# Optimization experiments

Hardware: AMD Instinct MI355X
Metric: run time of the kernel (lower is better)

## Reference

```python
import jax, jax.numpy as jnp
import numpy as np

N_NODES = 100000
N_EDGES = 1000000
D = 128          # node_dim == out_dim (embedding_dim)
EDGE_DIM = 10
NEG_SLOPE = 0.01  # torch leaky_relu default
EPS = 1e-16       # PyG softmax denominator eps


def _leaky(x):
    return jnp.where(x >= 0, x, NEG_SLOPE * x)


def setup_inputs() -> dict:
    key = jax.random.key(0)
    ks = jax.random.split(key, 12)
    s = lambda fan_in: 1.0 / np.sqrt(fan_in)
    return {
        "x": jax.random.normal(ks[0], (N_NODES, D), jnp.float32),
        "edge_index": jax.random.randint(ks[1], (2, N_EDGES), 0, N_NODES),
        "edge_attr": jax.random.normal(ks[2], (N_EDGES, EDGE_DIM), jnp.float32),
        # q: Linear(D, D, bias=False)
        "Wq": jax.random.uniform(ks[3], (D, D), jnp.float32, -s(D), s(D)),
        # k: Linear(EDGE_DIM, D, bias=False)
        "Wk": jax.random.uniform(ks[4], (D, EDGE_DIM), jnp.float32, -s(EDGE_DIM), s(EDGE_DIM)),
        # v: Linear(EDGE_DIM, D) with bias
        "Wv": jax.random.uniform(ks[5], (D, EDGE_DIM), jnp.float32, -s(EDGE_DIM), s(EDGE_DIM)),
        "bv": jax.random.uniform(ks[6], (D,), jnp.float32, -s(EDGE_DIM), s(EDGE_DIM)),
        # attn_score_layer: Linear(2D, D) -> ReLU -> Linear(D, 1)
        "W1": jax.random.uniform(ks[7], (D, 2 * D), jnp.float32, -s(2 * D), s(2 * D)),
        "b1": jax.random.uniform(ks[8], (D,), jnp.float32, -s(2 * D), s(2 * D)),
        "W2": jax.random.uniform(ks[9], (1, D), jnp.float32, -s(D), s(D)),
        "b2": jax.random.uniform(ks[10], (1,), jnp.float32, -s(D), s(D)),
    }


def reference(x, edge_index, edge_attr, Wq, Wk, Wv, bv, W1, b1, W2, b2):
    N = x.shape[0]
    tgt = edge_index[1]                       # destination node per edge [E]
    q = x @ Wq.T                              # [N, D] node queries
    x_i = q[tgt]                              # gather target queries [E, D]
    k = _leaky(edge_attr @ Wk.T)              # [E, D]
    v = _leaky(edge_attr @ Wv.T + bv)         # [E, D]
    h = jnp.concatenate([x_i, k], axis=-1)    # [E, 2D]
    scores = (jax.nn.relu(h @ W1.T + b1) @ W2.T + b2)[:, 0]  # [E]
    # segment softmax over edges grouped by target node (PyG softmax)
    smax = jax.ops.segment_max(scores, tgt, num_segments=N)  # [N]
    e = jnp.exp(scores - smax[tgt])
    denom = jax.ops.segment_sum(e, tgt, num_segments=N)
    attn = e / (denom[tgt] + EPS)             # [E]
    out = jax.ops.segment_sum(v * attn[:, None], tgt, num_segments=N)  # [N, D]
    return out, attn
```

## Files before the change

kernel.cpp:

```cpp
#include <hip/hip_runtime.h>
#include <stdint.h>

#define NN 100000
#define NE 1000000
#define NTILES (NE / 64)
#define NB_SCAN 391

typedef __attribute__((ext_vector_type(8))) short bf16x8;
typedef __attribute__((ext_vector_type(4))) float f32x4;

static const size_t OFF_W1K   = 0;
static const size_t OFF_W1BP  = 8192;
static const size_t OFF_MTB   = 40960;
static const size_t OFF_RP    = 73728;
static const size_t OFF_CUR   = 524288;
static const size_t OFF_PART  = 1048576;
static const size_t OFF_BSUM  = 1572864;
static const size_t OFF_BSUMX = 1576960;
static const size_t OFF_CNT   = 1581056;
static const size_t OFF_PT    = 2097152;
static const size_t OFF_EVALS = 10485760;
static const size_t OFF_EAS   = 14485760;
static const size_t OFF_SNODE = 34485760;

__device__ inline unsigned short f2bf(float f) {
    const unsigned int u = __float_as_uint(f);
    return (unsigned short)((u + 0x7fffu + ((u >> 16) & 1u)) >> 16);
}

__device__ inline unsigned int cvtpk(float lo, float hi) {
    unsigned int r;
    asm("v_cvt_pk_bf16_f32 %0, %1, %2" : "=v"(r) : "v"(lo), "v"(hi));
    return r;
}

__device__ inline float lk(float v) {
    return fmaxf(v, 0.f) + 0.01f * fminf(v, 0.f);
}

union BU { bf16x8 v; uint4 u; };

__global__ __launch_bounds__(128) void prep_kernel(
    const float* __restrict__ W1, const float* __restrict__ Wq,
    const float* __restrict__ Wk,
    unsigned short* __restrict__ w1k, unsigned short* __restrict__ w1bp,
    unsigned short* __restrict__ mtb)
{
    const int l = blockIdx.x;
    const int i = threadIdx.x;
    float acc = 0.f;
#pragma unroll 8
    for (int j = 0; j < 128; ++j)
        acc = fmaf(W1[i * 256 + j], Wq[j * 128 + l], acc);
    mtb[i * 128 + l] = f2bf(acc);
    if (i < 32)
        w1k[l * 32 + i] = (i < 10) ? f2bf(Wk[l * 10 + i]) : (unsigned short)0;
    const int m = l;
    const int j = (m & ~31) + 16 * ((m >> 2) & 1) + 4 * ((m >> 3) & 3) + (m & 3);
    w1bp[i * 128 + m] = f2bf(W1[i * 256 + 128 + j]);
}

__global__ __launch_bounds__(256) void node_score_kernel(
    const float* __restrict__ x, const unsigned short* __restrict__ mtb_g,
    const float* __restrict__ b1, unsigned short* __restrict__ s_node)
{
    __shared__ __align__(16) unsigned short mt_s[128 * 136];
    const int t = threadIdx.x;
    for (int idx = t; idx < 2048; idx += 256) {
        const uint4 v = ((const uint4*)mtb_g)[idx];
        const int row = idx >> 4, q = idx & 15;
        *(uint4*)&mt_s[row * 136 + q * 8] = v;
    }
    __syncthreads();

    const int lane = t & 63;
    const int wave = t >> 6;
    const int h    = lane >> 4;
    const int e15  = lane & 15;
    const int node = blockIdx.x * 64 + wave * 16 + e15;
    const int nc   = min(node, NN - 1);
    const int lds_base = e15 * 136 + h * 8;

    const f32x4 z4 = {0.f, 0.f, 0.f, 0.f};
    f32x4 acc[8];
#pragma unroll
    for (int g = 0; g < 8; ++g) acc[g] = z4;

#pragma unroll
    for (int s = 0; s < 4; ++s) {
        const float4 xa = *(const float4*)&x[(size_t)nc * 128 + s * 32 + h * 8];
        const float4 xb = *(const float4*)&x[(size_t)nc * 128 + s * 32 + h * 8 + 4];
        BU bx;
        bx.u.x = cvtpk(xa.x, xa.y);
        bx.u.y = cvtpk(xa.z, xa.w);
        bx.u.z = cvtpk(xb.x, xb.y);
        bx.u.w = cvtpk(xb.z, xb.w);
#pragma unroll
        for (int g = 0; g < 8; ++g) {
            const bf16x8 a = *(const bf16x8*)&mt_s[lds_base + g * (16 * 136) + s * 32];
            acc[g] = __builtin_amdgcn_mfma_f32_16x16x32_bf16(a, bx.v, acc[g], 0, 0, 0);
        }
    }

    if (node < NN) {
#pragma unroll
        for (int g = 0; g < 8; ++g) {
            const float4 bb = *(const float4*)&b1[g * 16 + h * 4];
            uint2 o2;
            o2.x = cvtpk(acc[g][0] + bb.x, acc[g][1] + bb.y);
            o2.y = cvtpk(acc[g][2] + bb.z, acc[g][3] + bb.w);
            *(uint2*)&s_node[(size_t)node * 128 + g * 16 + h * 4] = o2;
        }
    }
}

__global__ __launch_bounds__(256) void hist_kernel(
    const int* __restrict__ tgt, int* __restrict__ cnt)
{
    const int e = blockIdx.x * 256 + threadIdx.x;
    if (e < NE) atomicAdd(&cnt[tgt[e]], 1);
}

__global__ __launch_bounds__(256) void scan1_kernel(
    const int* __restrict__ cnt, int* __restrict__ part, int* __restrict__ bsum)
{
    __shared__ int s[256];
    const int t = threadIdx.x;
    const int idx = blockIdx.x * 256 + t;
    const int v = (idx < NN) ? cnt[idx] : 0;
    s[t] = v;
    __syncthreads();
    for (int off = 1; off < 256; off <<= 1) {
        const int u = (t >= off) ? s[t - off] : 0;
        __syncthreads();
        s[t] += u;
        __syncthreads();
    }
    part[idx] = s[t] - v;
    if (t == 255) bsum[blockIdx.x] = s[255];
}

__global__ __launch_bounds__(512) void scan2_kernel(
    const int* __restrict__ bsum, int* __restrict__ bsumx)
{
    __shared__ int s[512];
    const int t = threadIdx.x;
    const int v = (t < NB_SCAN) ? bsum[t] : 0;
    s[t] = v;
    __syncthreads();
    for (int off = 1; off < 512; off <<= 1) {
        const int u = (t >= off) ? s[t - off] : 0;
        __syncthreads();
        s[t] += u;
        __syncthreads();
    }
    if (t < NB_SCAN) bsumx[t] = s[t] - v;
}

__global__ __launch_bounds__(256) void scan3_kernel(
    const int* __restrict__ part, const int* __restrict__ bsumx,
    int* __restrict__ rowptr, int* __restrict__ cursor)
{
    const int idx = blockIdx.x * 256 + threadIdx.x;
    if (idx < NN) {
        const int rp = part[idx] + bsumx[idx >> 8];
        rowptr[idx] = rp;
        cursor[idx] = rp;
    }
    if (idx == 0) rowptr[NN] = NE;
}

__global__ __launch_bounds__(256) void fill_kernel(
    const int* __restrict__ tgt, int* __restrict__ cursor, int2* __restrict__ pt)
{
    const int e = blockIdx.x * 256 + threadIdx.x;
    if (e < NE) {
        const int tg = tgt[e];
        const int p  = atomicAdd(&cursor[tg], 1);
        pt[p] = make_int2(e, tg);
    }
}

__global__ __launch_bounds__(256) void edge_kernel(
    const float* __restrict__ edge_attr, const int2* __restrict__ pt,
    const unsigned short* __restrict__ w1k_g, const unsigned short* __restrict__ w1bp_g,
    const float* __restrict__ W2, const float* __restrict__ b2,
    const unsigned short* __restrict__ s_node,
    float* __restrict__ e_vals, unsigned int* __restrict__ eas)
{
    __shared__ __align__(16) unsigned short w1b_s[128 * 136];

    const int t = threadIdx.x;
    for (int idx = t; idx < 2048; idx += 256) {
        const uint4 v = ((const uint4*)w1bp_g)[idx];
        const int row = idx >> 4, q = idx & 15;
        *(uint4*)&w1b_s[row * 136 + q * 8] = v;
    }

    const int lane = t & 63;
    const int wave = t >> 6;
    const int h    = lane >> 4;
    const int e15  = lane & 15;

    bf16x8 a1[8];
#pragma unroll
    for (int f = 0; f < 8; ++f)
        a1[f] = *(const bf16x8*)&w1k_g[(f * 16 + e15) * 32 + h * 8];
    const float b2v = b2[0];

    __syncthreads();

    const int lds_base = e15 * 136 + h * 8;
    const int cstep    = gridDim.x * 64;

    int c = blockIdx.x * 64 + wave * 16 + e15;

    int2 ptc = pt[min(c, NE - 1)];
    int2 ptn = pt[min(c + cstep, NE - 1)];

    uint2 sn[8];
#pragma unroll
    for (int g = 0; g < 8; ++g)
        sn[g] = *(const uint2*)&s_node[(size_t)ptc.y * 128 + g * 16 + h * 4];

    float ea0 = 0.f, ea1 = 0.f, ea2 = 0.f, ea3 = 0.f, ea4 = 0.f;
    float ea5 = 0.f, ea6 = 0.f, ea7 = 0.f, ea8 = 0.f, ea9 = 0.f;
    {
        const float* pa = edge_attr + (size_t)ptc.x * 10;
        if (h == 0) {
            const float2 u0 = *(const float2*)(pa + 0);
            const float2 u1 = *(const float2*)(pa + 2);
            const float2 u2 = *(const float2*)(pa + 4);
            const float2 u3 = *(const float2*)(pa + 6);
            ea0 = u0.x; ea1 = u0.y; ea2 = u1.x; ea3 = u1.y;
            ea4 = u2.x; ea5 = u2.y; ea6 = u3.x; ea7 = u3.y;
        } else if (h == 1) {
            const float2 u4 = *(const float2*)(pa + 8);
            ea8 = u4.x; ea9 = u4.y;
        }
    }

    for (int tile = blockIdx.x; tile < NTILES; tile += gridDim.x, c += cstep) {
        const int2 ptn2 = pt[min(c + 2 * cstep, NE - 1)];
        uint2 sn_n[8];
#pragma unroll
        for (int g = 0; g < 8; ++g)
            sn_n[g] = *(const uint2*)&s_node[(size_t)ptn.y * 128 + g * 16 + h * 4];
        float en0 = 0.f, en1 = 0.f, en2 = 0.f, en3 = 0.f, en4 = 0.f;
        float en5 = 0.f, en6 = 0.f, en7 = 0.f, en8 = 0.f, en9 = 0.f;
        {
            const float* pa = edge_attr + (size_t)ptn.x * 10;
            if (h == 0) {
                const float2 u0 = *(const float2*)(pa + 0);
                const float2 u1 = *(const float2*)(pa + 2);
                const float2 u2 = *(const float2*)(pa + 4);
                const float2 u3 = *(const float2*)(pa + 6);
                en0 = u0.x; en1 = u0.y; en2 = u1.x; en3 = u1.y;
                en4 = u2.x; en5 = u2.y; en6 = u3.x; en7 = u3.y;
            } else if (h == 1) {
                const float2 u4 = *(const float2*)(pa + 8);
                en8 = u4.x; en9 = u4.y;
            }
        }

        bf16x8 b1 = (bf16x8){0, 0, 0, 0, 0, 0, 0, 0};
        {
            unsigned int* po = eas + (size_t)c * 5;
            if (h == 0) {
                BU bu;
                bu.u.x = cvtpk(ea0, ea1);
                bu.u.y = cvtpk(ea2, ea3);
                bu.u.z = cvtpk(ea4, ea5);
                bu.u.w = cvtpk(ea6, ea7);
                b1 = bu.v;
                po[0] = bu.u.x; po[1] = bu.u.y; po[2] = bu.u.z; po[3] = bu.u.w;
            } else if (h == 1) {
                BU bu;
                bu.u.x = cvtpk(ea8, ea9);
                bu.u.y = 0; bu.u.z = 0; bu.u.w = 0;
                b1 = bu.v;
                po[4] = bu.u.x;
            }
        }

        const f32x4 z4 = {0.f, 0.f, 0.f, 0.f};
        f32x4 acc1[8];
#pragma unroll
        for (int f = 0; f < 8; ++f)
            acc1[f] = __builtin_amdgcn_mfma_f32_16x16x32_bf16(a1[f], b1, z4, 0, 0, 0);

        bf16x8 pb[4];
#pragma unroll
        for (int s = 0; s < 4; ++s) {
            BU bu;
            bu.u.x = cvtpk(lk(acc1[2 * s][0]), lk(acc1[2 * s][1]));
            bu.u.y = cvtpk(lk(acc1[2 * s][2]), lk(acc1[2 * s][3]));
            bu.u.z = cvtpk(lk(acc1[2 * s + 1][0]), lk(acc1[2 * s + 1][1]));
            bu.u.w = cvtpk(lk(acc1[2 * s + 1][2]), lk(acc1[2 * s + 1][3]));
            pb[s] = bu.v;
        }

        float p = 0.f;
#pragma unroll
        for (int g2 = 0; g2 < 4; ++g2) {
            const int gA = 2 * g2, gB = 2 * g2 + 1;
            f32x4 accA = z4, accB = z4;
#pragma unroll
            for (int s = 0; s < 4; ++s) {
                const bf16x8 a2A = *(const bf16x8*)&w1b_s[lds_base + gA * (16 * 136) + s * 32];
                const bf16x8 a2B = *(const bf16x8*)&w1b_s[lds_base + gB * (16 * 136) + s * 32];
                accA = __builtin_amdgcn_mfma_f32_16x16x32_bf16(a2A, pb[s], accA, 0, 0, 0);
                accB = __builtin_amdgcn_mfma_f32_16x16x32_bf16(a2B, pb[s], accB, 0, 0, 0);
            }
            const float4 w2A = *(const float4*)&W2[gA * 16 + h * 4];
            const float4 w2B = *(const float4*)&W2[gB * 16 + h * 4];
            const uint2 svA = sn[gA], svB = sn[gB];
            p = fmaf(fmaxf(accA[0] + __uint_as_float(svA.x << 16), 0.f), w2A.x, p);
            p = fmaf(fmaxf(accA[1] + __uint_as_float(svA.x & 0xffff0000u), 0.f), w2A.y, p);
            p = fmaf(fmaxf(accA[2] + __uint_as_float(svA.y << 16), 0.f), w2A.z, p);
            p = fmaf(fmaxf(accA[3] + __uint_as_float(svA.y & 0xffff0000u), 0.f), w2A.w, p);
            p = fmaf(fmaxf(accB[0] + __uint_as_float(svB.x << 16), 0.f), w2B.x, p);
            p = fmaf(fmaxf(accB[1] + __uint_as_float(svB.x & 0xffff0000u), 0.f), w2B.y, p);
            p = fmaf(fmaxf(accB[2] + __uint_as_float(svB.y << 16), 0.f), w2B.z, p);
            p = fmaf(fmaxf(accB[3] + __uint_as_float(svB.y & 0xffff0000u), 0.f), w2B.w, p);
        }
        p += __shfl_xor(p, 16);
        p += __shfl_xor(p, 32);
        if (lane < 16)
            e_vals[c - e15 + lane] = __expf(p + b2v);

        ptc = ptn; ptn = ptn2;
#pragma unroll
        for (int g = 0; g < 8; ++g) sn[g] = sn_n[g];
        ea0 = en0; ea1 = en1; ea2 = en2; ea3 = en3; ea4 = en4;
        ea5 = en5; ea6 = en6; ea7 = en7; ea8 = en8; ea9 = en9;
    }
}

__global__ __launch_bounds__(256) void gather_kernel(
    const int* __restrict__ rowptr, const int2* __restrict__ pt,
    const float* __restrict__ e_vals, const unsigned int* __restrict__ eas,
    const float* __restrict__ Wv, const float* __restrict__ bv,
    float* __restrict__ out, float* __restrict__ attn_out)
{
    const int t    = threadIdx.x;
    const int lane = t & 63;
    const int wave = t >> 6;
    const int node = blockIdx.x * 4 + wave;
    const int d0   = lane * 2;

    float wv0[10], wv1[10];
#pragma unroll
    for (int c = 0; c < 10; ++c) {
        wv0[c] = Wv[d0 * 10 + c];
        wv1[c] = Wv[d0 * 10 + 10 + c];
    }
    const float bv0 = bv[d0], bv1 = bv[d0 + 1];

    const int start = rowptr[node];
    const int end   = rowptr[node + 1];

    float part = 0.f;
    for (int c = start + lane; c < end; c += 64) part += e_vals[c];
    part += __shfl_xor(part, 1);
    part += __shfl_xor(part, 2);
    part += __shfl_xor(part, 4);
    part += __shfl_xor(part, 8);
    part += __shfl_xor(part, 16);
    part += __shfl_xor(part, 32);
    const float inv = 1.f / (part + 1e-16f);

    float acc0 = 0.f, acc1 = 0.f;
    for (int c0 = start; c0 < end; c0 += 64) {
        const int m = min(64, end - c0);
        unsigned int w0 = 0, w1 = 0, w2 = 0, w3 = 0, w4 = 0;
        float evl = 0.f;
        if (lane < m) {
            const size_t cc = (size_t)(c0 + lane);
            const int ee = pt[cc].x;
            evl = e_vals[cc];
            attn_out[ee] = evl * inv;
            const unsigned int* pe = eas + cc * 5;
            w0 = pe[0]; w1 = pe[1]; w2 = pe[2]; w3 = pe[3]; w4 = pe[4];
        }
        const float r0 = __uint_as_float(w0 << 16), r1 = __uint_as_float(w0 & 0xffff0000u);
        const float r2 = __uint_as_float(w1 << 16), r3 = __uint_as_float(w1 & 0xffff0000u);
        const float r4 = __uint_as_float(w2 << 16), r5 = __uint_as_float(w2 & 0xffff0000u);
        const float r6 = __uint_as_float(w3 << 16), r7 = __uint_as_float(w3 & 0xffff0000u);
        const float r8 = __uint_as_float(w4 << 16), r9 = __uint_as_float(w4 & 0xffff0000u);
#pragma unroll 2
        for (int d = 0; d < m; ++d) {
            const float ad = __shfl(evl, d) * inv;
            const float c0v = __shfl(r0, d), c1v = __shfl(r1, d);
            const float c2v = __shfl(r2, d), c3v = __shfl(r3, d);
            const float c4v = __shfl(r4, d), c5v = __shfl(r5, d);
            const float c6v = __shfl(r6, d), c7v = __shfl(r7, d);
            const float c8v = __shfl(r8, d), c9v = __shfl(r9, d);
            float a0 = bv0, a1 = bv1;
            a0 = fmaf(c0v, wv0[0], a0); a1 = fmaf(c0v, wv1[0], a1);
            a0 = fmaf(c1v, wv0[1], a0); a1 = fmaf(c1v, wv1[1], a1);
            a0 = fmaf(c2v, wv0[2], a0); a1 = fmaf(c2v, wv1[2], a1);
            a0 = fmaf(c3v, wv0[3], a0); a1 = fmaf(c3v, wv1[3], a1);
            a0 = fmaf(c4v, wv0[4], a0); a1 = fmaf(c4v, wv1[4], a1);
            a0 = fmaf(c5v, wv0[5], a0); a1 = fmaf(c5v, wv1[5], a1);
            a0 = fmaf(c6v, wv0[6], a0); a1 = fmaf(c6v, wv1[6], a1);
            a0 = fmaf(c7v, wv0[7], a0); a1 = fmaf(c7v, wv1[7], a1);
            a0 = fmaf(c8v, wv0[8], a0); a1 = fmaf(c8v, wv1[8], a1);
            a0 = fmaf(c9v, wv0[9], a0); a1 = fmaf(c9v, wv1[9], a1);
            const float v0 = (a0 >= 0.f) ? a0 : 0.01f * a0;
            const float v1 = (a1 >= 0.f) ? a1 : 0.01f * a1;
            acc0 = fmaf(ad, v0, acc0);
            acc1 = fmaf(ad, v1, acc1);
        }
    }
    *(float2*)&out[(size_t)node * 128 + d0] = make_float2(acc0, acc1);
}

extern "C" void kernel_launch(void* const* d_in, const int* in_sizes, int n_in,
                              void* d_out, int out_size, void* d_ws, size_t ws_size,
                              hipStream_t stream)
{
    const float* x         = (const float*)d_in[0];
    const int*   eidx      = (const int*)d_in[1];
    const float* edge_attr = (const float*)d_in[2];
    const float* Wq        = (const float*)d_in[3];
    const float* Wk        = (const float*)d_in[4];
    const float* Wv        = (const float*)d_in[5];
    const float* bv        = (const float*)d_in[6];
    const float* W1        = (const float*)d_in[7];
    const float* b1        = (const float*)d_in[8];
    const float* W2        = (const float*)d_in[9];
    const float* b2        = (const float*)d_in[10];
    const int*   tgt       = eidx + NE;

    char* ws = (char*)d_ws;
    unsigned short* w1k    = (unsigned short*)(ws + OFF_W1K);
    unsigned short* w1bp   = (unsigned short*)(ws + OFF_W1BP);
    unsigned short* mtb    = (unsigned short*)(ws + OFF_MTB);
    int*            rowptr = (int*)(ws + OFF_RP);
    int*            cursor = (int*)(ws + OFF_CUR);
    int*            part   = (int*)(ws + OFF_PART);
    int*            bsum   = (int*)(ws + OFF_BSUM);
    int*            bsumx  = (int*)(ws + OFF_BSUMX);
    int*            cnt    = (int*)(ws + OFF_CNT);
    int2*           pt     = (int2*)(ws + OFF_PT);
    float*          e_vals = (float*)(ws + OFF_EVALS);
    unsigned int*   eas    = (unsigned int*)(ws + OFF_EAS);
    unsigned short* s_node = (unsigned short*)(ws + OFF_SNODE);

    float* out      = (float*)d_out;
    float* attn_out = out + (size_t)NN * 128;

    hipMemsetAsync(cnt, 0, (size_t)NN * sizeof(int), stream);

    prep_kernel<<<128, 128, 0, stream>>>(W1, Wq, Wk, w1k, w1bp, mtb);
    node_score_kernel<<<(NN + 63) / 64, 256, 0, stream>>>(x, mtb, b1, s_node);
    hist_kernel<<<(NE + 255) / 256, 256, 0, stream>>>(tgt, cnt);
    scan1_kernel<<<NB_SCAN, 256, 0, stream>>>(cnt, part, bsum);
    scan2_kernel<<<1, 512, 0, stream>>>(bsum, bsumx);
    scan3_kernel<<<NB_SCAN, 256, 0, stream>>>(part, bsumx, rowptr, cursor);
    fill_kernel<<<(NE + 255) / 256, 256, 0, stream>>>(tgt, cursor, pt);
    edge_kernel<<<768, 256, 0, stream>>>(edge_attr, pt, w1k, w1bp, W2, b2,
                                         s_node, e_vals, eas);
    gather_kernel<<<NN / 4, 256, 0, stream>>>(rowptr, pt, e_vals, eas,
                                              Wv, bv, out, attn_out);
}
```

Before: 353.3 us.

## Split gather into denom, attn and MFMA edge-tile value scatter kernels

Replaces the per-node gather kernel, which recomputed the value projection with scalar FMAs and wave shuffles, with three kernels. The first computes inverse denominators per node and zeroes output rows that span tiles, the second writes attention per edge, and the third computes the value projection for 64-edge tiles with bf16 MFMA. Per-node sums are reduced from LDS, with plain stores for nodes inside one tile and atomics for nodes that cross tile boundaries. This aims to use matrix cores and balance work across edges instead of nodes, at the cost of bf16 Wv precision, extra launches, an extra attention buffer, and atomics.

Measured after the change: 329.0 us. -6.9%, faster.

```diff
diff --git a/kernel.cpp b/kernel.cpp
--- a/kernel.cpp
+++ b/kernel.cpp
@@ -10,9 +10,10 @@
 typedef __attribute__((ext_vector_type(4))) float f32x4;
 
 static const size_t OFF_W1K   = 0;
-static const size_t OFF_W1BP  = 8192;
-static const size_t OFF_MTB   = 40960;
-static const size_t OFF_RP    = 73728;
+static const size_t OFF_WVK   = 8192;
+static const size_t OFF_W1BP  = 16384;
+static const size_t OFF_MTB   = 49152;
+static const size_t OFF_RP    = 81920;
 static const size_t OFF_CUR   = 524288;
 static const size_t OFF_PART  = 1048576;
 static const size_t OFF_BSUM  = 1572864;
@@ -20,8 +21,9 @@
 static const size_t OFF_CNT   = 1581056;
 static const size_t OFF_PT    = 2097152;
 static const size_t OFF_EVALS = 10485760;
-static const size_t OFF_EAS   = 14485760;
-static const size_t OFF_SNODE = 34485760;
+static const size_t OFF_ATTNS = 14485760;
+static const size_t OFF_EAS   = 18485760;
+static const size_t OFF_SNODE = 38485760;
 
 __device__ inline unsigned short f2bf(float f) {
     const unsigned int u = __float_as_uint(f);
@@ -42,9 +44,9 @@
 
 __global__ __launch_bounds__(128) void prep_kernel(
     const float* __restrict__ W1, const float* __restrict__ Wq,
-    const float* __restrict__ Wk,
-    unsigned short* __restrict__ w1k, unsigned short* __restrict__ w1bp,
-    unsigned short* __restrict__ mtb)
+    const float* __restrict__ Wk, const float* __restrict__ Wv,
+    unsigned short* __restrict__ w1k, unsigned short* __restrict__ wvk,
+    unsigned short* __restrict__ w1bp, unsigned short* __restrict__ mtb)
 {
     const int l = blockIdx.x;
     const int i = threadIdx.x;
@@ -53,8 +55,10 @@
     for (int j = 0; j < 128; ++j)
         acc = fmaf(W1[i * 256 + j], Wq[j * 128 + l], acc);
     mtb[i * 128 + l] = f2bf(acc);
-    if (i < 32)
+    if (i < 32) {
         w1k[l * 32 + i] = (i < 10) ? f2bf(Wk[l * 10 + i]) : (unsigned short)0;
+        wvk[l * 32 + i] = (i < 10) ? f2bf(Wv[l * 10 + i]) : (unsigned short)0;
+    }
     const int m = l;
     const int j = (m & ~31) + 16 * ((m >> 2) & 1) + 4 * ((m >> 3) & 3) + (m & 3);
     w1bp[i * 128 + m] = f2bf(W1[i * 256 + 128 + j]);
@@ -337,83 +341,107 @@
     }
 }
 
-__global__ __launch_bounds__(256) void gather_kernel(
+__global__ __launch_bounds__(256) void denom_kernel(
+    const int* __restrict__ rowptr, const float* __restrict__ e_vals,
+    float* __restrict__ inv_denom, float* __restrict__ out)
+{
+    const int n = blockIdx.x * 256 + threadIdx.x;
+    if (n >= NN) return;
+    const int rs = rowptr[n], re = rowptr[n + 1];
+    float s = 0.f;
+    for (int c = rs; c < re; ++c) s += e_vals[c];
+    inv_denom[n] = 1.f / (s + 1e-16f);
+    if (re > rs && (rs >> 6) != ((re - 1) >> 6)) {
+        const float4 z = make_float4(0.f, 0.f, 0.f, 0.f);
+        float4* po = (float4*)&out[(size_t)n * 128];
+#pragma unroll 8
+        for (int q = 0; q < 32; ++q) po[q] = z;
+    }
+}
+
+__global__ __launch_bounds__(256) void attn_kernel(
+    const int2* __restrict__ pt, const float* __restrict__ e_vals,
+    const float* __restrict__ inv_denom,
+    float* __restrict__ attn_s, float* __restrict__ attn_out)
+{
+    const int c = blockIdx.x * 256 + threadIdx.x;
+    if (c >= NE) return;
+    const int2 p = pt[c];
+    const float a = e_vals[c] * inv_denom[p.y];
+    attn_s[c] = a;
+    attn_out[p.x] = a;
+}
+
+__global__ __launch_bounds__(256) void vscatter_kernel(
     const int* __restrict__ rowptr, const int2* __restrict__ pt,
-    const float* __restrict__ e_vals, const unsigned int* __restrict__ eas,
-    const float* __restrict__ Wv, const float* __restrict__ bv,
-    float* __restrict__ out, float* __restrict__ attn_out)
-{
+    const unsigned int* __restrict__ eas, const float* __restrict__ attn_s,
+    const unsigned short* __restrict__ wvk_g, const float* __restrict__ bv,
+    float* __restrict__ out)
+{
+    __shared__ __align__(16) float w_lds[64 * 132];
+
     const int t    = threadIdx.x;
     const int lane = t & 63;
-    const int wave = t >> 6;
-    const int node = blockIdx.x * 4 + wave;
-    const int d0   = lane * 2;
-
-    float wv0[10], wv1[10];
-#pragma unroll
-    for (int c = 0; c < 10; ++c) {
-        wv0[c] = Wv[d0 * 10 + c];
-        wv1[c] = Wv[d0 * 10 + 10 + c];
-    }
-    const float bv0 = bv[d0], bv1 = bv[d0 + 1];
-
-    const int start = rowptr[node];
-    const int end   = rowptr[node + 1];
-
-    float part = 0.f;
-    for (int c = start + lane; c < end; c += 64) part += e_vals[c];
-    part += __shfl_xor(part, 1);
-    part += __shfl_xor(part, 2);
-    part += __shfl_xor(part, 4);
-    part += __shfl_xor(part, 8);
-    part += __shfl_xor(part, 16);
-    part += __shfl_xor(part, 32);
-    const float inv = 1.f / (part + 1e-16f);
-
-    float acc0 = 0.f, acc1 = 0.f;
-    for (int c0 = start; c0 < end; c0 += 64) {
-        const int m = min(64, end - c0);
-        unsigned int w0 = 0, w1 = 0, w2 = 0, w3 = 0, w4 = 0;
-        float evl = 0.f;
-        if (lane < m) {
-            const size_t cc = (size_t)(c0 + lane);
-            const int ee = pt[cc].x;
-            evl = e_vals[cc];
-            attn_out[ee] = evl * inv;
-            const unsigned int* pe = eas + cc * 5;
-            w0 = pe[0]; w1 = pe[1]; w2 = pe[2]; w3 = pe[3]; w4 = pe[4];
-        }
-        const float r0 = __uint_as_float(w0 << 16), r1 = __uint_as_float(w0 & 0xffff0000u);
-        const float r2 = __uint_as_float(w1 << 16), r3 = __uint_as_float(w1 & 0xffff0000u);
-        const float r4 = __uint_as_float(w2 << 16), r5 = __uint_as_float(w2 & 0xffff0000u);
-        const float r6 = __uint_as_float(w3 << 16), r7 = __uint_as_float(w3 & 0xffff0000u);
-        const float r8 = __uint_as_float(w4 << 16), r9 = __uint_as_float(w4 & 0xffff0000u);
-#pragma unroll 2
-        for (int d = 0; d < m; ++d) {
-            const float ad = __shfl(evl, d) * inv;
-            const float c0v = __shfl(r0, d), c1v = __shfl(r1, d);
-            const float c2v = __shfl(r2, d), c3v = __shfl(r3, d);
-            const float c4v = __shfl(r4, d), c5v = __shfl(r5, d);
-            const float c6v = __shfl(r6, d), c7v = __shfl(r7, d);
-            const float c8v = __shfl(r8, d), c9v = __shfl(r9, d);
-            float a0 = bv0, a1 = bv1;
-            a0 = fmaf(c0v, wv0[0], a0); a1 = fmaf(c0v, wv1[0], a1);
-            a0 = fmaf(c1v, wv0[1], a0); a1 = fmaf(c1v, wv1[1], a1);
-            a0 = fmaf(c2v, wv0[2], a0); a1 = fmaf(c2v, wv1[2], a1);
-            a0 = fmaf(c3v, wv0[3], a0); a1 = fmaf(c3v, wv1[3], a1);
-            a0 = fmaf(c4v, wv0[4], a0); a1 = fmaf(c4v, wv1[4], a1);
-            a0 = fmaf(c5v, wv0[5], a0); a1 = fmaf(c5v, wv1[5], a1);
-            a0 = fmaf(c6v, wv0[6], a0); a1 = fmaf(c6v, wv1[6], a1);
-            a0 = fmaf(c7v, wv0[7], a0); a1 = fmaf(c7v, wv1[7], a1);
-            a0 = fmaf(c8v, wv0[8], a0); a1 = fmaf(c8v, wv1[8], a1);
-            a0 = fmaf(c9v, wv0[9], a0); a1 = fmaf(c9v, wv1[9], a1);
-            const float v0 = (a0 >= 0.f) ? a0 : 0.01f * a0;
-            const float v1 = (a1 >= 0.f) ? a1 : 0.01f * a1;
-            acc0 = fmaf(ad, v0, acc0);
-            acc1 = fmaf(ad, v1, acc1);
-        }
-    }
-    *(float2*)&out[(size_t)node * 128 + d0] = make_float2(acc0, acc1);
+    const int wv   = t >> 6;
+    const int h    = lane >> 4;
+    const int e15  = lane & 15;
+    const int base = blockIdx.x * 64;
+    const int c    = base + wv * 16 + e15;
+    const int el   = wv * 16 + e15;
+
+    bf16x8 av[8];
+#pragma unroll
+    for (int g = 0; g < 8; ++g)
+        av[g] = *(const bf16x8*)&wvk_g[(g * 16 + e15) * 32 + h * 8];
+
+    bf16x8 be = (bf16x8){0, 0, 0, 0, 0, 0, 0, 0};
+    {
+        const unsigned int* pe = eas + (size_t)c * 5;
+        if (h == 0) {
+            BU bu;
+            bu.u.x = pe[0]; bu.u.y = pe[1]; bu.u.z = pe[2]; bu.u.w = pe[3];
+            be = bu.v;
+        } else if (h == 1) {
+            BU bu;
+            bu.u.x = pe[4]; bu.u.y = 0; bu.u.z = 0; bu.u.w = 0;
+            be = bu.v;
+        }
+    }
+    const float at = attn_s[c];
+
+    const f32x4 z4 = {0.f, 0.f, 0.f, 0.f};
+#pragma unroll
+    for (int g = 0; g < 8; ++g) {
+        const f32x4 acc = __builtin_amdgcn_mfma_f32_16x16x32_bf16(av[g], be, z4, 0, 0, 0);
+        const float4 bb = *(const float4*)&bv[g * 16 + h * 4];
+        float4 w;
+        w.x = at * lk(acc[0] + bb.x);
+        w.y = at * lk(acc[1] + bb.y);
+        w.z = at * lk(acc[2] + bb.z);
+        w.w = at * lk(acc[3] + bb.w);
+        *(float4*)&w_lds[el * 132 + g * 16 + h * 4] = w;
+    }
+    __syncthreads();
+
+    const int n_lo = (blockIdx.x == 0) ? 0 : pt[base].y;
+    const int n_hi = (blockIdx.x == (int)gridDim.x - 1) ? (NN - 1) : pt[base + 64].y;
+
+    for (int nd = n_lo + wv; nd <= n_hi; nd += 4) {
+        const int rs = rowptr[nd], re = rowptr[nd + 1];
+        const int lo = max(rs, base), hi = min(re, base + 64);
+        float sx = 0.f, sy = 0.f;
+        for (int cc = lo; cc < hi; ++cc) {
+            const float2 v = *(const float2*)&w_lds[(cc - base) * 132 + lane * 2];
+            sx += v.x; sy += v.y;
+        }
+        float* po = &out[(size_t)nd * 128 + lane * 2];
+        if (rs >= base && re <= base + 64) {
+            *(float2*)po = make_float2(sx, sy);
+        } else {
+            atomicAdd(po, sx);
+            atomicAdd(po + 1, sy);
+        }
+    }
 }
 
 extern "C" void kernel_launch(void* const* d_in, const int* in_sizes, int n_in,
@@ -435,16 +463,19 @@
 
     char* ws = (char*)d_ws;
     unsigned short* w1k    = (unsigned short*)(ws + OFF_W1K);
+    unsigned short* wvk    = (unsigned short*)(ws + OFF_WVK);
     unsigned short* w1bp   = (unsigned short*)(ws + OFF_W1BP);
     unsigned short* mtb    = (unsigned short*)(ws + OFF_MTB);
     int*            rowptr = (int*)(ws + OFF_RP);
     int*            cursor = (int*)(ws + OFF_CUR);
+    float*          invd   = (float*)(ws + OFF_CUR);
     int*            part   = (int*)(ws + OFF_PART);
     int*            bsum   = (int*)(ws + OFF_BSUM);
     int*            bsumx  = (int*)(ws + OFF_BSUMX);
     int*            cnt    = (int*)(ws + OFF_CNT);
     int2*           pt     = (int2*)(ws + OFF_PT);
     float*          e_vals = (float*)(ws + OFF_EVALS);
+    float*          attn_s = (float*)(ws + OFF_ATTNS);
     unsigned int*   eas    = (unsigned int*)(ws + OFF_EAS);
     unsigned short* s_node = (unsigned short*)(ws + OFF_SNODE);
 
@@ -453,7 +484,7 @@
 
     hipMemsetAsync(cnt, 0, (size_t)NN * sizeof(int), stream);
 
-    prep_kernel<<<128, 128, 0, stream>>>(W1, Wq, Wk, w1k, w1bp, mtb);
+    prep_kernel<<<128, 128, 0, stream>>>(W1, Wq, Wk, Wv, w1k, wvk, w1bp, mtb);
     node_score_kernel<<<(NN + 63) / 64, 256, 0, stream>>>(x, mtb, b1, s_node);
     hist_kernel<<<(NE + 255) / 256, 256, 0, stream>>>(tgt, cnt);
     scan1_kernel<<<NB_SCAN, 256, 0, stream>>>(cnt, part, bsum);
@@ -462,6 +493,9 @@
     fill_kernel<<<(NE + 255) / 256, 256, 0, stream>>>(tgt, cursor, pt);
     edge_kernel<<<768, 256, 0, stream>>>(edge_attr, pt, w1k, w1bp, W2, b2,
                                          s_node, e_vals, eas);
-    gather_kernel<<<NN / 4, 256, 0, stream>>>(rowptr, pt, e_vals, eas,
-                                              Wv, bv, out, attn_out);
-}
+    denom_kernel<<<(NN + 255) / 256, 256, 0, stream>>>(rowptr, e_vals, invd, out);
+    attn_kernel<<<(NE + 255) / 256, 256, 0, stream>>>(pt, e_vals, invd,
+                                                      attn_s, attn_out);
+    vscatter_kernel<<<NTILES, 256, 0, stream>>>(rowptr, pt, eas, attn_s,
+                                                wvk, bv, out);
+}
```
